# Kernel tuning notes

Hardware: AMD Instinct MI355X
Metric: run time of the kernel (lower is better)

## Reference

```python
import jax, jax.numpy as jnp
import numpy as np

NUM_V, NUM_E, NNZ, F = 65536, 16384, 1048576, 128

# wavelet constructor: fixed [6, 17] dyadic-difference matrix from the source
def _wavelet_matrix(dtype):
    W = np.zeros((6, 17), dtype=np.float32)
    pairs = [(0, 0, 1), (1, 1, 2), (2, 2, 4), (3, 4, 8), (4, 8, 16)]
    for row, a, b in pairs:
        W[row, a] = 1.0
        W[row, b] = -1.0
    W[5, 16] = 1.0
    return jnp.asarray(W, dtype)


def setup_inputs() -> dict:
    key = jax.random.key(0)
    k1, k2, k3 = jax.random.split(key, 3)
    X = jax.random.normal(k1, (NUM_V, F), dtype=jnp.float32)
    vertex_ids = jax.random.randint(k2, (NNZ,), 0, NUM_V)
    edge_ids = jax.random.randint(k3, (NNZ,), 0, NUM_E)
    return {"X": X, "vertex_ids": vertex_ids, "edge_ids": edge_ids, "num_e": NUM_E}


def reference(X, vertex_ids, edge_ids, num_e):
    num_v, feat = X.shape
    ones = jnp.ones(vertex_ids.shape[0], X.dtype)
    deg_v = jax.ops.segment_sum(ones, vertex_ids, num_segments=num_v)
    deg_e = jax.ops.segment_sum(ones, edge_ids, num_segments=num_e)
    # nan_to_num(1/deg): zero where degree is zero
    inv_v = jnp.where(deg_v > 0, 1.0 / jnp.where(deg_v > 0, deg_v, 1.0), 0.0)
    inv_e = jnp.where(deg_e > 0, 1.0 / jnp.where(deg_e > 0, deg_e, 1.0), 0.0)

    def step(x, _):
        x_norm = x * inv_v[:, None]                                        # [V,F]
        edge_feat = jax.ops.segment_sum(x_norm[vertex_ids], edge_ids,
                                        num_segments=num_e)                # v2e sum [E,F]
        node_feat = jax.ops.segment_sum((edge_feat * inv_e[:, None])[edge_ids],
                                        vertex_ids, num_segments=num_v)    # e2v sum [V,F]
        return node_feat, node_feat

    _, node_levels = jax.lax.scan(step, X, None, length=16)                # [16,V,F]
    levels = jnp.concatenate([X[None], node_levels], axis=0)               # [17,V,F]
    W = _wavelet_matrix(X.dtype)                                           # [6,17]
    wav = jnp.einsum('ij,jnf->inf', W, levels)                             # [6,V,F]
    s = jnp.concatenate([jax.nn.relu(wav), jax.nn.relu(-wav)], axis=-1)    # [6,V,2F] (blis)
    return jnp.swapaxes(s, 0, 1)                                           # [V,6,2F]
```

## Files before the change

kernel.cpp:

```cpp
#include <hip/hip_runtime.h>
#include <hip/hip_fp16.h>

#define FEAT 128


__device__ inline float hlo(unsigned u) {
    unsigned short s = (unsigned short)(u & 0xFFFFu);
    __half h = *(__half*)&s;
    return __half2float(h);
}
__device__ inline float hhi(unsigned u) {
    unsigned short s = (unsigned short)(u >> 16);
    __half h = *(__half*)&s;
    return __half2float(h);
}
__device__ inline unsigned hpack(float a, float b) {
    __half ha = __float2half_rn(a), hb = __float2half_rn(b);
    unsigned short ua = *(unsigned short*)&ha, ub = *(unsigned short*)&hb;
    return (unsigned)ua | ((unsigned)ub << 16);
}

#if __has_builtin(__builtin_amdgcn_cvt_pk_f32_fp8) && __has_builtin(__builtin_amdgcn_cvt_pk_fp8_f32)
typedef float floatx2 __attribute__((ext_vector_type(2)));
__device__ inline void fp8x2_to_f32(unsigned lo16, float& a, float& b) {
    floatx2 r = __builtin_amdgcn_cvt_pk_f32_fp8((int)lo16, false);
    a = r.x;
    b = r.y;
}
__device__ inline unsigned f32_to_fp8x2(float a, float b) {
    return (unsigned)__builtin_amdgcn_cvt_pk_fp8_f32(a, b, 0, false) & 0xFFFFu;
}
#else
__device__ inline float fp8_dec1(unsigned u) {
    unsigned s = (u >> 7) & 1u, e = (u >> 3) & 15u, m = u & 7u;
    float v;
    if (e != 0) {
        unsigned bits = (s << 31) | ((e + 120u) << 23) | (m << 20);
        v = __uint_as_float(bits);
    } else {
        v = (float)m * 0.001953125f;
        if (s) v = -v;
    }
    return v;
}
__device__ inline void fp8x2_to_f32(unsigned lo16, float& a, float& b) {
    a = fp8_dec1(lo16 & 0xFFu);
    b = fp8_dec1((lo16 >> 8) & 0xFFu);
}
__device__ inline unsigned fp8_enc1(float x) {
    float ax = fabsf(x);
    unsigned s = (__float_as_uint(x) >> 31) << 7;
    if (ax >= 448.f) return s | 0x7Eu;
    if (ax < 0.0009765625f) return s;
    if (ax < 0.015625f) {
        unsigned m = (unsigned)__builtin_rintf(ax * 512.f);
        if (m > 7u) m = 7u;
        return s | m;
    }
    unsigned bits = __float_as_uint(ax);
    int e32 = (int)((bits >> 23) & 255u) - 127;
    unsigned mant = bits & 0x7FFFFFu;
    unsigned m3 = mant >> 20;
    unsigned rem = mant & 0xFFFFFu;
    if (rem > 0x80000u || (rem == 0x80000u && (m3 & 1u))) {
        m3++;
        if (m3 == 8u) { m3 = 0; e32++; }
    }
    if (e32 > 8) return s | 0x7Eu;
    return s | ((unsigned)(e32 + 7) << 3) | m3;
}
__device__ inline unsigned f32_to_fp8x2(float a, float b) {
    return fp8_enc1(a) | (fp8_enc1(b) << 8);
}
#endif


__global__ void count_deg(const int* __restrict__ vids, const int* __restrict__ eids,
                          int* __restrict__ deg_v, int* __restrict__ deg_e, int nnz) {
    int n = blockIdx.x * blockDim.x + threadIdx.x;
    if (n < nnz) {
        atomicAdd(&deg_v[vids[n]], 1);
        atomicAdd(&deg_e[eids[n]], 1);
    }
}

template <int N, int T, int CHUNK>
__global__ __launch_bounds__(T) void scan_pad(const int* __restrict__ deg,
                                              int* __restrict__ off,
                                              int* __restrict__ cur,
                                              float* __restrict__ inv) {
    __shared__ int partial[T];
    const int per = N / T;
    int tid = threadIdx.x;
    int base = tid * per;
    int dloc[per];
    int s = 0;
#pragma unroll
    for (int i = 0; i < per / 4; ++i) {
        int4 d4 = *(const int4*)(deg + base + 4 * i);
        dloc[4 * i] = d4.x; dloc[4 * i + 1] = d4.y;
        dloc[4 * i + 2] = d4.z; dloc[4 * i + 3] = d4.w;
        s += ((d4.x + CHUNK - 1) & ~(CHUNK - 1)) + ((d4.y + CHUNK - 1) & ~(CHUNK - 1)) +
             ((d4.z + CHUNK - 1) & ~(CHUNK - 1)) + ((d4.w + CHUNK - 1) & ~(CHUNK - 1));
    }
    partial[tid] = s;
    __syncthreads();
    for (int d = 1; d < T; d <<= 1) {
        int add = (tid >= d) ? partial[tid - d] : 0;
        __syncthreads();
        partial[tid] += add;
        __syncthreads();
    }
    int run = (tid > 0) ? partial[tid - 1] : 0;
#pragma unroll
    for (int i = 0; i < per / 4; ++i) {
        int o[4];
        float iv[4];
#pragma unroll
        for (int j = 0; j < 4; ++j) {
            int d = dloc[4 * i + j];
            o[j] = run;
            iv[j] = (d > 0) ? (1.0f / (float)d) : 0.0f;
            run += (d + CHUNK - 1) & ~(CHUNK - 1);
        }
        *(int4*)(off + base + 4 * i) = make_int4(o[0], o[1], o[2], o[3]);
        *(int4*)(cur + base + 4 * i) = make_int4(o[0], o[1], o[2], o[3]);
        *(float4*)(inv + base + 4 * i) = make_float4(iv[0], iv[1], iv[2], iv[3]);
    }
    if (tid == T - 1) off[N] = run;
}

__global__ void init_pad(int* __restrict__ nbrE, int nE, int dummyE,
                         int* __restrict__ nbrV, int nV, int dummyV,
                         unsigned* __restrict__ x8zero, unsigned* __restrict__ e8zero) {
    int i = blockIdx.x * 256 + threadIdx.x;
    if (i < nE) nbrE[i] = dummyE;
    if (i < nV) nbrV[i] = dummyV;
    if (i < 32) { x8zero[i] = 0u; e8zero[i] = 0u; }
}

__global__ void fill_csr(const int* __restrict__ vids, const int* __restrict__ eids,
                         int* __restrict__ cur_v, int* __restrict__ cur_e,
                         int* __restrict__ v_nbr_e, int* __restrict__ e_nbr_v, int nnz) {
    int n = blockIdx.x * blockDim.x + threadIdx.x;
    if (n < nnz) {
        int v = vids[n], e = eids[n];
        int p = atomicAdd(&cur_e[e], 1);
        e_nbr_v[p] = v;
        int q = atomicAdd(&cur_v[v], 1);
        v_nbr_e[q] = e;
    }
}

__global__ __launch_bounds__(256) void prescale(const float* __restrict__ X,
                                                const float* __restrict__ inv_v,
                                                unsigned* __restrict__ xs8) {
    int tid = blockIdx.x * 256 + threadIdx.x;
    int v = tid >> 5, d = tid & 31;
    float sc = inv_v[v];
    float4 x = *(const float4*)(X + (size_t)v * FEAT + 4 * d);
    unsigned lo = f32_to_fp8x2(x.x * sc, x.y * sc);
    unsigned hi = f32_to_fp8x2(x.z * sc, x.w * sc);
    xs8[(size_t)v * 32 + d] = lo | (hi << 16);
}

__global__ __launch_bounds__(256) void gather_v2e(const unsigned short* __restrict__ xs8,
                                                  const int* __restrict__ offs,
                                                  const int* __restrict__ nbr,
                                                  const float* __restrict__ inv_e,
                                                  unsigned short* __restrict__ es8, int nseg) {
    int seg = __builtin_amdgcn_readfirstlane(blockIdx.x * 4 + (threadIdx.x >> 6));
    if (seg >= nseg) return;
    int lane = threadIdx.x & 63;
    int p = offs[seg], pend = offs[seg + 1];
    float ax = 0.f, ay = 0.f;
    for (; p < pend; p += 8) {
        int4 c0 = *(const int4*)(nbr + p);
        int4 c1 = *(const int4*)(nbr + p + 4);
        unsigned r0 = xs8[(size_t)c0.x * 64 + lane];
        unsigned r1 = xs8[(size_t)c0.y * 64 + lane];
        unsigned r2 = xs8[(size_t)c0.z * 64 + lane];
        unsigned r3 = xs8[(size_t)c0.w * 64 + lane];
        unsigned r4 = xs8[(size_t)c1.x * 64 + lane];
        unsigned r5 = xs8[(size_t)c1.y * 64 + lane];
        unsigned r6 = xs8[(size_t)c1.z * 64 + lane];
        unsigned r7 = xs8[(size_t)c1.w * 64 + lane];
        float a, b;
        fp8x2_to_f32(r0, a, b); ax += a; ay += b;
        fp8x2_to_f32(r1, a, b); ax += a; ay += b;
        fp8x2_to_f32(r2, a, b); ax += a; ay += b;
        fp8x2_to_f32(r3, a, b); ax += a; ay += b;
        fp8x2_to_f32(r4, a, b); ax += a; ay += b;
        fp8x2_to_f32(r5, a, b); ax += a; ay += b;
        fp8x2_to_f32(r6, a, b); ax += a; ay += b;
        fp8x2_to_f32(r7, a, b); ax += a; ay += b;
    }
    float sc = inv_e[seg];
    es8[(size_t)seg * 64 + lane] = (unsigned short)f32_to_fp8x2(ax * sc, ay * sc);
}

__global__ __launch_bounds__(256) void gather_e2v(const unsigned short* __restrict__ es8,
                                                  const int* __restrict__ offs,
                                                  const int* __restrict__ nbr,
                                                  const float* __restrict__ inv_v,
                                                  unsigned short* __restrict__ xs8,
                                                  unsigned* __restrict__ ckpt, int nseg) {
    int wv = __builtin_amdgcn_readfirstlane(blockIdx.x * 4 + (threadIdx.x >> 6));
    int lane = threadIdx.x & 63;
    int seg0 = wv * 4;
    if (seg0 >= nseg) return;
    int p = offs[seg0];
#pragma unroll
    for (int i = 0; i < 4; ++i) {
        int s = seg0 + i;
        int pend = offs[s + 1];
        float ax = 0.f, ay = 0.f;
        for (; p < pend; p += 4) {
            int4 c0 = *(const int4*)(nbr + p);
            unsigned r0 = es8[(size_t)c0.x * 64 + lane];
            unsigned r1 = es8[(size_t)c0.y * 64 + lane];
            unsigned r2 = es8[(size_t)c0.z * 64 + lane];
            unsigned r3 = es8[(size_t)c0.w * 64 + lane];
            float a, b;
            fp8x2_to_f32(r0, a, b); ax += a; ay += b;
            fp8x2_to_f32(r1, a, b); ax += a; ay += b;
            fp8x2_to_f32(r2, a, b); ax += a; ay += b;
            fp8x2_to_f32(r3, a, b); ax += a; ay += b;
        }
        float sc = inv_v[s];
        float xl = ax * sc, xh = ay * sc;
        xs8[(size_t)s * 64 + lane] = (unsigned short)f32_to_fp8x2(xl, xh);
        if (ckpt) ckpt[(size_t)s * 1536 + lane] = hpack(xl, xh);
    }
}

__global__ __launch_bounds__(256) void wavelet_out(const float* __restrict__ X,
                                                   const int* __restrict__ deg_v,
                                                   float* __restrict__ out) {
    int tid = blockIdx.x * 256 + threadIdx.x;
    int v = tid >> 5;
    int f4 = (tid & 31) * 4;
    float* row = out + (size_t)v * 1536;
    const unsigned* rowu = (const unsigned*)row;
    float degf = (float)deg_v[v];
    float4 L0v = *(const float4*)(X + (size_t)v * FEAT + f4);
    float l0[4] = {L0v.x, L0v.y, L0v.z, L0v.w};
    float L[5][4];
#pragma unroll
    for (int s = 0; s < 5; ++s) {
        unsigned d0 = rowu[(s + 1) * 256 + (f4 >> 1)];
        unsigned d1 = rowu[(s + 1) * 256 + (f4 >> 1) + 1];
        L[s][0] = hlo(d0) * degf;
        L[s][1] = hhi(d0) * degf;
        L[s][2] = hlo(d1) * degf;
        L[s][3] = hhi(d1) * degf;
    }
    float wv[6][4];
#pragma unroll
    for (int j = 0; j < 4; ++j) {
        wv[0][j] = l0[j] - L[0][j];
        wv[1][j] = L[0][j] - L[1][j];
        wv[2][j] = L[1][j] - L[2][j];
        wv[3][j] = L[2][j] - L[3][j];
        wv[4][j] = L[3][j] - L[4][j];
        wv[5][j] = L[4][j];
    }
    __syncthreads();
#pragma unroll
    for (int r = 0; r < 6; ++r) {
        float4 pp, mm;
        pp.x = fmaxf(wv[r][0], 0.f); mm.x = fmaxf(-wv[r][0], 0.f);
        pp.y = fmaxf(wv[r][1], 0.f); mm.y = fmaxf(-wv[r][1], 0.f);
        pp.z = fmaxf(wv[r][2], 0.f); mm.z = fmaxf(-wv[r][2], 0.f);
        pp.w = fmaxf(wv[r][3], 0.f); mm.w = fmaxf(-wv[r][3], 0.f);
        *(float4*)(row + r * 256 + f4) = pp;
        *(float4*)(row + r * 256 + 128 + f4) = mm;
    }
}


extern "C" void kernel_launch(void* const* d_in, const int* in_sizes, int n_in,
                              void* d_out, int out_size, void* d_ws, size_t ws_size,
                              hipStream_t stream) {
    const float* X = (const float*)d_in[0];
    const int* vids = (const int*)d_in[1];
    const int* eids = (const int*)d_in[2];
    const int NNZ = in_sizes[1];
    const int V = in_sizes[0] / FEAT;
    const int E = 16384;
    float* out = (float*)d_out;

    const int NBRE_CAP = NNZ + E * 8;
    const int NBRV_CAP = NNZ + V * 4;

    char* w = (char*)d_ws;
    size_t o = 0;
    auto take = [&](size_t bytes) {
        void* p = (void*)(w + o);
        o = (o + bytes + 255) & ~(size_t)255;
        return p;
    };
    int* deg_v = (int*)take((size_t)(V + E) * 4);
    int* deg_e = deg_v + V;
    int* off_e = (int*)take((size_t)(E + 1) * 4);
    int* off_v = (int*)take((size_t)(V + 1) * 4);
    int* cur_e = (int*)take((size_t)E * 4);
    int* cur_v = (int*)take((size_t)V * 4);
    float* inv_e = (float*)take((size_t)E * 4);
    float* inv_v = (float*)take((size_t)V * 4);
    int* e_nbr_v = (int*)take((size_t)NBRE_CAP * 4);
    int* v_nbr_e = (int*)take((size_t)NBRV_CAP * 4);
    unsigned* xs8 = (unsigned*)take((size_t)(V + 1) * 32 * 4);
    unsigned* es8 = (unsigned*)take((size_t)(E + 1) * 32 * 4);
    (void)ws_size;
    (void)n_in;
    (void)out_size;

    hipMemsetAsync(deg_v, 0, (size_t)(V + E) * 4, stream);
    count_deg<<<(NNZ + 255) / 256, 256, 0, stream>>>(vids, eids, deg_v, deg_e, NNZ);

    scan_pad<16384, 1024, 8><<<1, 1024, 0, stream>>>(deg_e, off_e, cur_e, inv_e);
    scan_pad<65536, 1024, 4><<<1, 1024, 0, stream>>>(deg_v, off_v, cur_v, inv_v);

    {
        int mx = NBRV_CAP > NBRE_CAP ? NBRV_CAP : NBRE_CAP;
        init_pad<<<(mx + 255) / 256, 256, 0, stream>>>(e_nbr_v, NBRE_CAP, V,
                                                       v_nbr_e, NBRV_CAP, E,
                                                       xs8 + (size_t)V * 32,
                                                       es8 + (size_t)E * 32);
    }

    fill_csr<<<(NNZ + 255) / 256, 256, 0, stream>>>(vids, eids, cur_v, cur_e,
                                                    v_nbr_e, e_nbr_v, NNZ);

    prescale<<<V * 32 / 256, 256, 0, stream>>>(X, inv_v, xs8);

    for (int k = 1; k <= 16; ++k) {
        gather_v2e<<<E / 4, 256, 0, stream>>>((const unsigned short*)xs8, off_e,
                                              e_nbr_v, inv_e, (unsigned short*)es8, E);
        unsigned* ck = nullptr;
        if (k == 1) ck = (unsigned*)out + 1 * 256;
        else if (k == 2) ck = (unsigned*)out + 2 * 256;
        else if (k == 4) ck = (unsigned*)out + 3 * 256;
        else if (k == 8) ck = (unsigned*)out + 4 * 256;
        else if (k == 16) ck = (unsigned*)out + 5 * 256;
        gather_e2v<<<V / 16, 256, 0, stream>>>((const unsigned short*)es8, off_v,
                                               v_nbr_e, inv_v, (unsigned short*)xs8, ck, V);
    }

    wavelet_out<<<V * 32 / 256, 256, 0, stream>>>(X, deg_v, out);
}
```

Baseline: 1.059 ms.

## Gather fp8 rows with wide per-lane loads and cross-lane shuffle reduction

Before, each lane read a 2-byte fp8 pair from every neighbor row. Now lane groups split the neighbors: in v2e each of eight 8-lane groups reads one neighbor's 128-byte row as 16-byte loads, and in e2v four 16-lane groups use 8-byte loads. Partial sums are combined with xor shuffles and a subset of lanes writes the packed result with wide stores. This cuts load instruction count and moves wider, better-coalesced transactions, at the cost of shuffle reductions and more accumulator registers.

```diff
diff --git a/kernel.cpp b/kernel.cpp
--- a/kernel.cpp
+++ b/kernel.cpp
@@ -22,13 +22,18 @@
 
 #if __has_builtin(__builtin_amdgcn_cvt_pk_f32_fp8) && __has_builtin(__builtin_amdgcn_cvt_pk_fp8_f32)
 typedef float floatx2 __attribute__((ext_vector_type(2)));
-__device__ inline void fp8x2_to_f32(unsigned lo16, float& a, float& b) {
-    floatx2 r = __builtin_amdgcn_cvt_pk_f32_fp8((int)lo16, false);
-    a = r.x;
-    b = r.y;
-}
-__device__ inline unsigned f32_to_fp8x2(float a, float b) {
-    return (unsigned)__builtin_amdgcn_cvt_pk_fp8_f32(a, b, 0, false) & 0xFFFFu;
+__device__ inline void fp8x2lo(unsigned u, float& a, float& b) {
+    floatx2 r = __builtin_amdgcn_cvt_pk_f32_fp8((int)u, false);
+    a = r.x; b = r.y;
+}
+__device__ inline void fp8x2hi(unsigned u, float& a, float& b) {
+    floatx2 r = __builtin_amdgcn_cvt_pk_f32_fp8((int)u, true);
+    a = r.x; b = r.y;
+}
+__device__ inline unsigned fp8x4(float a, float b, float c, float d) {
+    int w = __builtin_amdgcn_cvt_pk_fp8_f32(a, b, 0, false);
+    w = __builtin_amdgcn_cvt_pk_fp8_f32(c, d, w, true);
+    return (unsigned)w;
 }
 #else
 __device__ inline float fp8_dec1(unsigned u) {
@@ -43,9 +48,13 @@
     }
     return v;
 }
-__device__ inline void fp8x2_to_f32(unsigned lo16, float& a, float& b) {
-    a = fp8_dec1(lo16 & 0xFFu);
-    b = fp8_dec1((lo16 >> 8) & 0xFFu);
+__device__ inline void fp8x2lo(unsigned u, float& a, float& b) {
+    a = fp8_dec1(u & 0xFFu);
+    b = fp8_dec1((u >> 8) & 0xFFu);
+}
+__device__ inline void fp8x2hi(unsigned u, float& a, float& b) {
+    a = fp8_dec1((u >> 16) & 0xFFu);
+    b = fp8_dec1((u >> 24) & 0xFFu);
 }
 __device__ inline unsigned fp8_enc1(float x) {
     float ax = fabsf(x);
@@ -69,8 +78,8 @@
     if (e32 > 8) return s | 0x7Eu;
     return s | ((unsigned)(e32 + 7) << 3) | m3;
 }
-__device__ inline unsigned f32_to_fp8x2(float a, float b) {
-    return fp8_enc1(a) | (fp8_enc1(b) << 8);
+__device__ inline unsigned fp8x4(float a, float b, float c, float d) {
+    return fp8_enc1(a) | (fp8_enc1(b) << 8) | (fp8_enc1(c) << 16) | (fp8_enc1(d) << 24);
 }
 #endif
 
@@ -159,54 +168,65 @@
     int v = tid >> 5, d = tid & 31;
     float sc = inv_v[v];
     float4 x = *(const float4*)(X + (size_t)v * FEAT + 4 * d);
-    unsigned lo = f32_to_fp8x2(x.x * sc, x.y * sc);
-    unsigned hi = f32_to_fp8x2(x.z * sc, x.w * sc);
-    xs8[(size_t)v * 32 + d] = lo | (hi << 16);
-}
-
-__global__ __launch_bounds__(256) void gather_v2e(const unsigned short* __restrict__ xs8,
+    xs8[(size_t)v * 32 + d] = fp8x4(x.x * sc, x.y * sc, x.z * sc, x.w * sc);
+}
+
+__global__ __launch_bounds__(256) void gather_v2e(const char* __restrict__ xs8b,
                                                   const int* __restrict__ offs,
                                                   const int* __restrict__ nbr,
                                                   const float* __restrict__ inv_e,
-                                                  unsigned short* __restrict__ es8, int nseg) {
+                                                  char* __restrict__ es8b, int nseg) {
     int seg = __builtin_amdgcn_readfirstlane(blockIdx.x * 4 + (threadIdx.x >> 6));
     if (seg >= nseg) return;
     int lane = threadIdx.x & 63;
+    int q = lane & 7, g = lane >> 3;
     int p = offs[seg], pend = offs[seg + 1];
-    float ax = 0.f, ay = 0.f;
+    float acc[16];
+#pragma unroll
+    for (int j = 0; j < 16; ++j) acc[j] = 0.f;
     for (; p < pend; p += 8) {
         int4 c0 = *(const int4*)(nbr + p);
         int4 c1 = *(const int4*)(nbr + p + 4);
-        unsigned r0 = xs8[(size_t)c0.x * 64 + lane];
-        unsigned r1 = xs8[(size_t)c0.y * 64 + lane];
-        unsigned r2 = xs8[(size_t)c0.z * 64 + lane];
-        unsigned r3 = xs8[(size_t)c0.w * 64 + lane];
-        unsigned r4 = xs8[(size_t)c1.x * 64 + lane];
-        unsigned r5 = xs8[(size_t)c1.y * 64 + lane];
-        unsigned r6 = xs8[(size_t)c1.z * 64 + lane];
-        unsigned r7 = xs8[(size_t)c1.w * 64 + lane];
+        int i0 = (g & 2) ? ((g & 1) ? c0.w : c0.z) : ((g & 1) ? c0.y : c0.x);
+        int i1 = (g & 2) ? ((g & 1) ? c1.w : c1.z) : ((g & 1) ? c1.y : c1.x);
+        int idx = (g & 4) ? i1 : i0;
+        uint4 r = *(const uint4*)(xs8b + (((size_t)(unsigned)idx) << 7) + (q << 4));
         float a, b;
-        fp8x2_to_f32(r0, a, b); ax += a; ay += b;
-        fp8x2_to_f32(r1, a, b); ax += a; ay += b;
-        fp8x2_to_f32(r2, a, b); ax += a; ay += b;
-        fp8x2_to_f32(r3, a, b); ax += a; ay += b;
-        fp8x2_to_f32(r4, a, b); ax += a; ay += b;
-        fp8x2_to_f32(r5, a, b); ax += a; ay += b;
-        fp8x2_to_f32(r6, a, b); ax += a; ay += b;
-        fp8x2_to_f32(r7, a, b); ax += a; ay += b;
-    }
-    float sc = inv_e[seg];
-    es8[(size_t)seg * 64 + lane] = (unsigned short)f32_to_fp8x2(ax * sc, ay * sc);
-}
-
-__global__ __launch_bounds__(256) void gather_e2v(const unsigned short* __restrict__ es8,
+        fp8x2lo(r.x, a, b); acc[0] += a;  acc[1] += b;
+        fp8x2hi(r.x, a, b); acc[2] += a;  acc[3] += b;
+        fp8x2lo(r.y, a, b); acc[4] += a;  acc[5] += b;
+        fp8x2hi(r.y, a, b); acc[6] += a;  acc[7] += b;
+        fp8x2lo(r.z, a, b); acc[8] += a;  acc[9] += b;
+        fp8x2hi(r.z, a, b); acc[10] += a; acc[11] += b;
+        fp8x2lo(r.w, a, b); acc[12] += a; acc[13] += b;
+        fp8x2hi(r.w, a, b); acc[14] += a; acc[15] += b;
+    }
+#pragma unroll
+    for (int j = 0; j < 16; ++j) acc[j] += __shfl_xor(acc[j], 8, 64);
+#pragma unroll
+    for (int j = 0; j < 16; ++j) acc[j] += __shfl_xor(acc[j], 16, 64);
+#pragma unroll
+    for (int j = 0; j < 16; ++j) acc[j] += __shfl_xor(acc[j], 32, 64);
+    if (lane < 8) {
+        float sc = inv_e[seg];
+        uint4 o;
+        o.x = fp8x4(acc[0] * sc, acc[1] * sc, acc[2] * sc, acc[3] * sc);
+        o.y = fp8x4(acc[4] * sc, acc[5] * sc, acc[6] * sc, acc[7] * sc);
+        o.z = fp8x4(acc[8] * sc, acc[9] * sc, acc[10] * sc, acc[11] * sc);
+        o.w = fp8x4(acc[12] * sc, acc[13] * sc, acc[14] * sc, acc[15] * sc);
+        *(uint4*)(es8b + (((size_t)seg) << 7) + (lane << 4)) = o;
+    }
+}
+
+__global__ __launch_bounds__(256) void gather_e2v(const char* __restrict__ es8b,
                                                   const int* __restrict__ offs,
                                                   const int* __restrict__ nbr,
                                                   const float* __restrict__ inv_v,
-                                                  unsigned short* __restrict__ xs8,
+                                                  char* __restrict__ xs8b,
                                                   unsigned* __restrict__ ckpt, int nseg) {
     int wv = __builtin_amdgcn_readfirstlane(blockIdx.x * 4 + (threadIdx.x >> 6));
     int lane = threadIdx.x & 63;
+    int q = lane & 15, g = lane >> 4;
     int seg0 = wv * 4;
     if (seg0 >= nseg) return;
     int p = offs[seg0];
@@ -214,23 +234,40 @@
     for (int i = 0; i < 4; ++i) {
         int s = seg0 + i;
         int pend = offs[s + 1];
-        float ax = 0.f, ay = 0.f;
+        float acc[8];
+#pragma unroll
+        for (int j = 0; j < 8; ++j) acc[j] = 0.f;
         for (; p < pend; p += 4) {
-            int4 c0 = *(const int4*)(nbr + p);
-            unsigned r0 = es8[(size_t)c0.x * 64 + lane];
-            unsigned r1 = es8[(size_t)c0.y * 64 + lane];
-            unsigned r2 = es8[(size_t)c0.z * 64 + lane];
-            unsigned r3 = es8[(size_t)c0.w * 64 + lane];
+            int4 c = *(const int4*)(nbr + p);
+            int idx = (g & 2) ? ((g & 1) ? c.w : c.z) : ((g & 1) ? c.y : c.x);
+            uint2 r = *(const uint2*)(es8b + (((size_t)(unsigned)idx) << 7) + (q << 3));
             float a, b;
-            fp8x2_to_f32(r0, a, b); ax += a; ay += b;
-            fp8x2_to_f32(r1, a, b); ax += a; ay += b;
-            fp8x2_to_f32(r2, a, b); ax += a; ay += b;
-            fp8x2_to_f32(r3, a, b); ax += a; ay += b;
+            fp8x2lo(r.x, a, b); acc[0] += a; acc[1] += b;
+            fp8x2hi(r.x, a, b); acc[2] += a; acc[3] += b;
+            fp8x2lo(r.y, a, b); acc[4] += a; acc[5] += b;
+            fp8x2hi(r.y, a, b); acc[6] += a; acc[7] += b;
         }
-        float sc = inv_v[s];
-        float xl = ax * sc, xh = ay * sc;
-        xs8[(size_t)s * 64 + lane] = (unsigned short)f32_to_fp8x2(xl, xh);
-        if (ckpt) ckpt[(size_t)s * 1536 + lane] = hpack(xl, xh);
+#pragma unroll
+        for (int j = 0; j < 8; ++j) acc[j] += __shfl_xor(acc[j], 16, 64);
+#pragma unroll
+        for (int j = 0; j < 8; ++j) acc[j] += __shfl_xor(acc[j], 32, 64);
+        if (lane < 16) {
+            float sc = inv_v[s];
+            float f0 = acc[0] * sc, f1 = acc[1] * sc, f2 = acc[2] * sc, f3 = acc[3] * sc;
+            float f4 = acc[4] * sc, f5 = acc[5] * sc, f6 = acc[6] * sc, f7 = acc[7] * sc;
+            uint2 o;
+            o.x = fp8x4(f0, f1, f2, f3);
+            o.y = fp8x4(f4, f5, f6, f7);
+            *(uint2*)(xs8b + (((size_t)s) << 7) + (lane << 3)) = o;
+            if (ckpt) {
+                uint4 h;
+                h.x = hpack(f0, f1);
+                h.y = hpack(f2, f3);
+                h.z = hpack(f4, f5);
+                h.w = hpack(f6, f7);
+                *(uint4*)(ckpt + (size_t)s * 1536 + lane * 4) = h;
+            }
+        }
     }
 }
 
@@ -336,16 +373,16 @@
     prescale<<<V * 32 / 256, 256, 0, stream>>>(X, inv_v, xs8);
 
     for (int k = 1; k <= 16; ++k) {
-        gather_v2e<<<E / 4, 256, 0, stream>>>((const unsigned short*)xs8, off_e,
-                                              e_nbr_v, inv_e, (unsigned short*)es8, E);
+        gather_v2e<<<E / 4, 256, 0, stream>>>((const char*)xs8, off_e, e_nbr_v,
+                                              inv_e, (char*)es8, E);
         unsigned* ck = nullptr;
         if (k == 1) ck = (unsigned*)out + 1 * 256;
         else if (k == 2) ck = (unsigned*)out + 2 * 256;
         else if (k == 4) ck = (unsigned*)out + 3 * 256;
         else if (k == 8) ck = (unsigned*)out + 4 * 256;
         else if (k == 16) ck = (unsigned*)out + 5 * 256;
-        gather_e2v<<<V / 16, 256, 0, stream>>>((const unsigned short*)es8, off_v,
-                                               v_nbr_e, inv_v, (unsigned short*)xs8, ck, V);
+        gather_e2v<<<V / 16, 256, 0, stream>>>((const char*)es8, off_v, v_nbr_e,
+                                               inv_v, (char*)xs8, ck, V);
     }
 
     wavelet_out<<<V * 32 / 256, 256, 0, stream>>>(X, deg_v, out);
```

Result: slower. 1.140 ms (+7.6%).

## Bucket edge neighbor lists by vertex range and merge scan/pad setup kernels

Applied to the files above, without the earlier changes.

Edge CSR neighbor lists are now sorted into 8 buckets by vertex id range (v>>13), so each edge's gathers in the v2e pass touch vertex rows in roughly ascending order. The aim is better L2/TLB locality on the 16 repeated gathers. The two scans and the padding-init kernel are merged into one two-block kernel, which removes launches and a full-buffer fill; pad slots are now written only where needed. Output and checkpoint stores become nontemporal. The cost is an 8x larger per-edge counter array and a serial per-thread inner loop in the scan.

```diff
diff --git a/kernel.cpp b/kernel.cpp
--- a/kernel.cpp
+++ b/kernel.cpp
@@ -2,6 +2,8 @@
 #include <hip/hip_fp16.h>
 
 #define FEAT 128
+
+typedef float f32x4 __attribute__((ext_vector_type(4)));
 
 
 __device__ inline float hlo(unsigned u) {
@@ -76,76 +78,103 @@
 
 
 __global__ void count_deg(const int* __restrict__ vids, const int* __restrict__ eids,
-                          int* __restrict__ deg_v, int* __restrict__ deg_e, int nnz) {
+                          int* __restrict__ deg_v, int* __restrict__ deg_eb, int nnz) {
     int n = blockIdx.x * blockDim.x + threadIdx.x;
     if (n < nnz) {
-        atomicAdd(&deg_v[vids[n]], 1);
-        atomicAdd(&deg_e[eids[n]], 1);
-    }
-}
-
-template <int N, int T, int CHUNK>
-__global__ __launch_bounds__(T) void scan_pad(const int* __restrict__ deg,
-                                              int* __restrict__ off,
-                                              int* __restrict__ cur,
-                                              float* __restrict__ inv) {
-    __shared__ int partial[T];
-    const int per = N / T;
+        int v = vids[n], e = eids[n];
+        atomicAdd(&deg_v[v], 1);
+        atomicAdd(&deg_eb[e * 8 + (v >> 13)], 1);
+    }
+}
+
+__global__ __launch_bounds__(1024) void scan_both(
+    const int* __restrict__ deg_v, const int* __restrict__ deg_eb,
+    int* __restrict__ off_e, int* __restrict__ cur_eb, float* __restrict__ inv_e,
+    int* __restrict__ e_nbr_v,
+    int* __restrict__ off_v, int* __restrict__ cur_v, float* __restrict__ inv_v,
+    int* __restrict__ v_nbr_e,
+    unsigned* __restrict__ xs8d, unsigned* __restrict__ es8d, int V, int E) {
+    __shared__ int partial[1024];
     int tid = threadIdx.x;
-    int base = tid * per;
-    int dloc[per];
-    int s = 0;
-#pragma unroll
-    for (int i = 0; i < per / 4; ++i) {
-        int4 d4 = *(const int4*)(deg + base + 4 * i);
-        dloc[4 * i] = d4.x; dloc[4 * i + 1] = d4.y;
-        dloc[4 * i + 2] = d4.z; dloc[4 * i + 3] = d4.w;
-        s += ((d4.x + CHUNK - 1) & ~(CHUNK - 1)) + ((d4.y + CHUNK - 1) & ~(CHUNK - 1)) +
-             ((d4.z + CHUNK - 1) & ~(CHUNK - 1)) + ((d4.w + CHUNK - 1) & ~(CHUNK - 1));
-    }
-    partial[tid] = s;
-    __syncthreads();
-    for (int d = 1; d < T; d <<= 1) {
-        int add = (tid >= d) ? partial[tid - d] : 0;
+    if (blockIdx.x == 0) {
+        const int per = 16;
+        int base = tid * per;
+        int degs[per];
+        int s = 0;
+#pragma unroll
+        for (int i = 0; i < per; ++i) {
+            int d = 0;
+#pragma unroll
+            for (int b = 0; b < 8; ++b) d += deg_eb[(base + i) * 8 + b];
+            degs[i] = d;
+            s += (d + 7) & ~7;
+        }
+        partial[tid] = s;
         __syncthreads();
-        partial[tid] += add;
+        for (int dd = 1; dd < 1024; dd <<= 1) {
+            int add = (tid >= dd) ? partial[tid - dd] : 0;
+            __syncthreads();
+            partial[tid] += add;
+            __syncthreads();
+        }
+        int run = (tid > 0) ? partial[tid - 1] : 0;
+#pragma unroll
+        for (int i = 0; i < per; ++i) {
+            int e = base + i, d = degs[i];
+            off_e[e] = run;
+            inv_e[e] = (d > 0) ? (1.0f / (float)d) : 0.0f;
+            int b0 = run;
+#pragma unroll
+            for (int b = 0; b < 8; ++b) {
+                cur_eb[e * 8 + b] = b0;
+                b0 += deg_eb[e * 8 + b];
+            }
+            int pad = (d + 7) & ~7;
+            for (int j = d; j < pad; ++j) e_nbr_v[run + j] = V;
+            run += pad;
+        }
+        if (tid == 1023) off_e[E] = run;
+        if (tid < 32) es8d[(size_t)E * 32 + tid] = 0u;
+    } else {
+        const int per = 64;
+        int base = tid * per;
+        int s = 0;
+        for (int i = 0; i < per; i += 4) {
+            int4 d4 = *(const int4*)(deg_v + base + i);
+            s += ((d4.x + 3) & ~3) + ((d4.y + 3) & ~3) + ((d4.z + 3) & ~3) +
+                 ((d4.w + 3) & ~3);
+        }
+        partial[tid] = s;
         __syncthreads();
-    }
-    int run = (tid > 0) ? partial[tid - 1] : 0;
-#pragma unroll
-    for (int i = 0; i < per / 4; ++i) {
-        int o[4];
-        float iv[4];
-#pragma unroll
-        for (int j = 0; j < 4; ++j) {
-            int d = dloc[4 * i + j];
-            o[j] = run;
-            iv[j] = (d > 0) ? (1.0f / (float)d) : 0.0f;
-            run += (d + CHUNK - 1) & ~(CHUNK - 1);
-        }
-        *(int4*)(off + base + 4 * i) = make_int4(o[0], o[1], o[2], o[3]);
-        *(int4*)(cur + base + 4 * i) = make_int4(o[0], o[1], o[2], o[3]);
-        *(float4*)(inv + base + 4 * i) = make_float4(iv[0], iv[1], iv[2], iv[3]);
-    }
-    if (tid == T - 1) off[N] = run;
-}
-
-__global__ void init_pad(int* __restrict__ nbrE, int nE, int dummyE,
-                         int* __restrict__ nbrV, int nV, int dummyV,
-                         unsigned* __restrict__ x8zero, unsigned* __restrict__ e8zero) {
-    int i = blockIdx.x * 256 + threadIdx.x;
-    if (i < nE) nbrE[i] = dummyE;
-    if (i < nV) nbrV[i] = dummyV;
-    if (i < 32) { x8zero[i] = 0u; e8zero[i] = 0u; }
+        for (int dd = 1; dd < 1024; dd <<= 1) {
+            int add = (tid >= dd) ? partial[tid - dd] : 0;
+            __syncthreads();
+            partial[tid] += add;
+            __syncthreads();
+        }
+        int run = (tid > 0) ? partial[tid - 1] : 0;
+        for (int i = 0; i < per; ++i) {
+            int v = base + i;
+            int d = deg_v[v];
+            off_v[v] = run;
+            cur_v[v] = run;
+            inv_v[v] = (d > 0) ? (1.0f / (float)d) : 0.0f;
+            int pad = (d + 3) & ~3;
+            for (int j = d; j < pad; ++j) v_nbr_e[run + j] = E;
+            run += pad;
+        }
+        if (tid == 1023) off_v[V] = run;
+        if (tid < 32) xs8d[(size_t)V * 32 + tid] = 0u;
+    }
 }
 
 __global__ void fill_csr(const int* __restrict__ vids, const int* __restrict__ eids,
-                         int* __restrict__ cur_v, int* __restrict__ cur_e,
+                         int* __restrict__ cur_v, int* __restrict__ cur_eb,
                          int* __restrict__ v_nbr_e, int* __restrict__ e_nbr_v, int nnz) {
     int n = blockIdx.x * blockDim.x + threadIdx.x;
     if (n < nnz) {
         int v = vids[n], e = eids[n];
-        int p = atomicAdd(&cur_e[e], 1);
+        int p = atomicAdd(&cur_eb[e * 8 + (v >> 13)], 1);
         e_nbr_v[p] = v;
         int q = atomicAdd(&cur_v[v], 1);
         v_nbr_e[q] = e;
@@ -164,11 +193,11 @@
     xs8[(size_t)v * 32 + d] = lo | (hi << 16);
 }
 
-__global__ __launch_bounds__(256) void gather_v2e(const unsigned short* __restrict__ xs8,
-                                                  const int* __restrict__ offs,
-                                                  const int* __restrict__ nbr,
-                                                  const float* __restrict__ inv_e,
-                                                  unsigned short* __restrict__ es8, int nseg) {
+__global__ __launch_bounds__(256) void k_v2e(const unsigned short* __restrict__ xs8,
+                                             const int* __restrict__ offs,
+                                             const int* __restrict__ nbr,
+                                             const float* __restrict__ inv_e,
+                                             unsigned short* __restrict__ es8, int nseg) {
     int seg = __builtin_amdgcn_readfirstlane(blockIdx.x * 4 + (threadIdx.x >> 6));
     if (seg >= nseg) return;
     int lane = threadIdx.x & 63;
@@ -199,12 +228,12 @@
     es8[(size_t)seg * 64 + lane] = (unsigned short)f32_to_fp8x2(ax * sc, ay * sc);
 }
 
-__global__ __launch_bounds__(256) void gather_e2v(const unsigned short* __restrict__ es8,
-                                                  const int* __restrict__ offs,
-                                                  const int* __restrict__ nbr,
-                                                  const float* __restrict__ inv_v,
-                                                  unsigned short* __restrict__ xs8,
-                                                  unsigned* __restrict__ ckpt, int nseg) {
+__global__ __launch_bounds__(256) void k_e2v(const unsigned short* __restrict__ es8,
+                                             const int* __restrict__ offs,
+                                             const int* __restrict__ nbr,
+                                             const float* __restrict__ inv_v,
+                                             unsigned short* __restrict__ xs8,
+                                             unsigned* __restrict__ ckpt, int nseg) {
     int wv = __builtin_amdgcn_readfirstlane(blockIdx.x * 4 + (threadIdx.x >> 6));
     int lane = threadIdx.x & 63;
     int seg0 = wv * 4;
@@ -216,11 +245,11 @@
         int pend = offs[s + 1];
         float ax = 0.f, ay = 0.f;
         for (; p < pend; p += 4) {
-            int4 c0 = *(const int4*)(nbr + p);
-            unsigned r0 = es8[(size_t)c0.x * 64 + lane];
-            unsigned r1 = es8[(size_t)c0.y * 64 + lane];
-            unsigned r2 = es8[(size_t)c0.z * 64 + lane];
-            unsigned r3 = es8[(size_t)c0.w * 64 + lane];
+            int4 c = *(const int4*)(nbr + p);
+            unsigned r0 = es8[(size_t)c.x * 64 + lane];
+            unsigned r1 = es8[(size_t)c.y * 64 + lane];
+            unsigned r2 = es8[(size_t)c.z * 64 + lane];
+            unsigned r3 = es8[(size_t)c.w * 64 + lane];
             float a, b;
             fp8x2_to_f32(r0, a, b); ax += a; ay += b;
             fp8x2_to_f32(r1, a, b); ax += a; ay += b;
@@ -230,7 +259,8 @@
         float sc = inv_v[s];
         float xl = ax * sc, xh = ay * sc;
         xs8[(size_t)s * 64 + lane] = (unsigned short)f32_to_fp8x2(xl, xh);
-        if (ckpt) ckpt[(size_t)s * 1536 + lane] = hpack(xl, xh);
+        if (ckpt)
+            __builtin_nontemporal_store(hpack(xl, xh), &ckpt[(size_t)s * 1536 + lane]);
     }
 }
 
@@ -268,13 +298,13 @@
     __syncthreads();
 #pragma unroll
     for (int r = 0; r < 6; ++r) {
-        float4 pp, mm;
+        f32x4 pp, mm;
         pp.x = fmaxf(wv[r][0], 0.f); mm.x = fmaxf(-wv[r][0], 0.f);
         pp.y = fmaxf(wv[r][1], 0.f); mm.y = fmaxf(-wv[r][1], 0.f);
         pp.z = fmaxf(wv[r][2], 0.f); mm.z = fmaxf(-wv[r][2], 0.f);
         pp.w = fmaxf(wv[r][3], 0.f); mm.w = fmaxf(-wv[r][3], 0.f);
-        *(float4*)(row + r * 256 + f4) = pp;
-        *(float4*)(row + r * 256 + 128 + f4) = mm;
+        __builtin_nontemporal_store(pp, (f32x4*)(row + r * 256 + f4));
+        __builtin_nontemporal_store(mm, (f32x4*)(row + r * 256 + 128 + f4));
     }
 }
 
@@ -289,6 +319,7 @@
     const int V = in_sizes[0] / FEAT;
     const int E = 16384;
     float* out = (float*)d_out;
+    unsigned* out_u = (unsigned*)d_out;
 
     const int NBRE_CAP = NNZ + E * 8;
     const int NBRV_CAP = NNZ + V * 4;
@@ -300,11 +331,11 @@
         o = (o + bytes + 255) & ~(size_t)255;
         return p;
     };
-    int* deg_v = (int*)take((size_t)(V + E) * 4);
-    int* deg_e = deg_v + V;
+    int* deg_v = (int*)take((size_t)(V + E * 8) * 4);
+    int* deg_eb = deg_v + V;
     int* off_e = (int*)take((size_t)(E + 1) * 4);
     int* off_v = (int*)take((size_t)(V + 1) * 4);
-    int* cur_e = (int*)take((size_t)E * 4);
+    int* cur_eb = (int*)take((size_t)E * 8 * 4);
     int* cur_v = (int*)take((size_t)V * 4);
     float* inv_e = (float*)take((size_t)E * 4);
     float* inv_v = (float*)take((size_t)V * 4);
@@ -316,36 +347,28 @@
     (void)n_in;
     (void)out_size;
 
-    hipMemsetAsync(deg_v, 0, (size_t)(V + E) * 4, stream);
-    count_deg<<<(NNZ + 255) / 256, 256, 0, stream>>>(vids, eids, deg_v, deg_e, NNZ);
-
-    scan_pad<16384, 1024, 8><<<1, 1024, 0, stream>>>(deg_e, off_e, cur_e, inv_e);
-    scan_pad<65536, 1024, 4><<<1, 1024, 0, stream>>>(deg_v, off_v, cur_v, inv_v);
-
-    {
-        int mx = NBRV_CAP > NBRE_CAP ? NBRV_CAP : NBRE_CAP;
-        init_pad<<<(mx + 255) / 256, 256, 0, stream>>>(e_nbr_v, NBRE_CAP, V,
-                                                       v_nbr_e, NBRV_CAP, E,
-                                                       xs8 + (size_t)V * 32,
-                                                       es8 + (size_t)E * 32);
-    }
-
-    fill_csr<<<(NNZ + 255) / 256, 256, 0, stream>>>(vids, eids, cur_v, cur_e,
+    hipMemsetAsync(deg_v, 0, (size_t)(V + E * 8) * 4, stream);
+    count_deg<<<(NNZ + 255) / 256, 256, 0, stream>>>(vids, eids, deg_v, deg_eb, NNZ);
+
+    scan_both<<<2, 1024, 0, stream>>>(deg_v, deg_eb, off_e, cur_eb, inv_e, e_nbr_v,
+                                      off_v, cur_v, inv_v, v_nbr_e, xs8, es8, V, E);
+
+    fill_csr<<<(NNZ + 255) / 256, 256, 0, stream>>>(vids, eids, cur_v, cur_eb,
                                                     v_nbr_e, e_nbr_v, NNZ);
 
     prescale<<<V * 32 / 256, 256, 0, stream>>>(X, inv_v, xs8);
 
     for (int k = 1; k <= 16; ++k) {
-        gather_v2e<<<E / 4, 256, 0, stream>>>((const unsigned short*)xs8, off_e,
-                                              e_nbr_v, inv_e, (unsigned short*)es8, E);
+        k_v2e<<<E / 4, 256, 0, stream>>>((const unsigned short*)xs8, off_e, e_nbr_v,
+                                         inv_e, (unsigned short*)es8, E);
         unsigned* ck = nullptr;
-        if (k == 1) ck = (unsigned*)out + 1 * 256;
-        else if (k == 2) ck = (unsigned*)out + 2 * 256;
-        else if (k == 4) ck = (unsigned*)out + 3 * 256;
-        else if (k == 8) ck = (unsigned*)out + 4 * 256;
-        else if (k == 16) ck = (unsigned*)out + 5 * 256;
-        gather_e2v<<<V / 16, 256, 0, stream>>>((const unsigned short*)es8, off_v,
-                                               v_nbr_e, inv_v, (unsigned short*)xs8, ck, V);
+        if (k == 1) ck = out_u + 1 * 256;
+        else if (k == 2) ck = out_u + 2 * 256;
+        else if (k == 4) ck = out_u + 3 * 256;
+        else if (k == 8) ck = out_u + 4 * 256;
+        else if (k == 16) ck = out_u + 5 * 256;
+        k_e2v<<<V / 16, 256, 0, stream>>>((const unsigned short*)es8, off_v, v_nbr_e,
+                                          inv_v, (unsigned short*)xs8, ck, V);
     }
 
     wavelet_out<<<V * 32 / 256, 256, 0, stream>>>(X, deg_v, out);
```

After: 1.187 ms. 12.1% more time.
